# Optimization experiments

Measured on AMD Instinct MI355X. Metric: run time of the kernel, lower is better.

The kernel has to match this reference:

```python
import jax, jax.numpy as jnp
import numpy as np
from jax import lax

EPS_LN = 1e-5
EPS_NORM = 1e-12
NUM_HEADS = 8
KV_HEADS = 2
REP = NUM_HEADS // KV_HEADS


def _layernorm_c(x, w, b):
    # WithBias LayerNorm over channel dim; x: [b,c,h,w]
    mu = x.mean(axis=1, keepdims=True)
    var = ((x - mu) ** 2).mean(axis=1, keepdims=True)
    return (x - mu) / jnp.sqrt(var + EPS_LN) * w[None, :, None, None] + b[None, :, None, None]


def _conv1x1(x, w):
    # x: [b,c,h,w], w: [o,c]
    return jnp.einsum('bchw,oc->bohw', x, w)


def _dwconv3x3(x, w):
    # depthwise 3x3, SAME padding; w: [C,1,3,3]
    C = x.shape[1]
    return lax.conv_general_dilated(
        x, w, window_strides=(1, 1), padding='SAME',
        dimension_numbers=('NCHW', 'OIHW', 'NCHW'), feature_group_count=C)


def _l2norm(x):
    # normalize over last axis (torch F.normalize semantics)
    n = jnp.sqrt(jnp.sum(x * x, axis=-1, keepdims=True))
    return x / jnp.maximum(n, EPS_NORM)


def setup_inputs() -> dict:
    key = jax.random.key(0)
    ks = jax.random.split(key, 8)
    b, dim, h, w = 4, 192, 256, 256
    kv_ch = 2 * dim // REP  # 96
    return {
        'x': jax.random.normal(ks[0], (b, dim, h, w), jnp.float32),
        'ln_w': jnp.ones((dim,), jnp.float32),
        'ln_b': jnp.zeros((dim,), jnp.float32),
        'q_w': jax.random.normal(ks[1], (dim, dim), jnp.float32) * 0.02,
        'q_dw': jax.random.normal(ks[2], (dim, 1, 3, 3), jnp.float32) * 0.1,
        'kv_w': jax.random.normal(ks[3], (kv_ch, dim), jnp.float32) * 0.02,
        'kv_dw': jax.random.normal(ks[4], (kv_ch, 1, 3, 3), jnp.float32) * 0.1,
        'proj_w': jax.random.normal(ks[5], (dim, dim), jnp.float32) * 0.02,
        'temperature': jnp.ones((NUM_HEADS, 1, 1), jnp.float32),
    }


def reference(x, ln_w, ln_b, q_w, q_dw, kv_w, kv_dw, proj_w, temperature):
    b, c, h, w = x.shape
    xn = _layernorm_c(x, ln_w, ln_b)
    q = _dwconv3x3(_conv1x1(xn, q_w), q_dw)            # [b, c, h, w]
    kv = _dwconv3x3(_conv1x1(xn, kv_w), kv_dw)         # [b, 2c/rep, h, w]
    k, v = jnp.split(kv, 2, axis=1)
    hw = h * w
    ch = c // NUM_HEADS
    q = q.reshape(b, NUM_HEADS, ch, hw)
    k = k.reshape(b, KV_HEADS, ch, hw)
    v = v.reshape(b, KV_HEADS, ch, hw)
    k = jnp.repeat(k, REP, axis=1)                     # repeat_kv
    v = jnp.repeat(v, REP, axis=1)
    q = _l2norm(q)
    k = _l2norm(k)
    attn = jnp.einsum('bhcn,bhdn->bhcd', q, k) * temperature[None]
    attn = jax.nn.softmax(attn, axis=-1)
    out = jnp.einsum('bhcd,bhdn->bhcn', attn, v)
    out = out.reshape(b, c, h, w)
    return _conv1x1(out, proj_w)
```

## Files before the change

kernel.cpp:

```cpp
#include <hip/hip_runtime.h>
#include <hip/hip_bf16.h>
#include <stdint.h>

#define HW    65536
#define NB    4
#define CIN   192
#define OYC   288
#define BSTR  200

__device__ __forceinline__ float bflo(unsigned u){ return __uint_as_float(u << 16); }
__device__ __forceinline__ float bfhi(unsigned u){ return __uint_as_float(u & 0xffff0000u); }
__device__ __forceinline__ float bf2f(__hip_bfloat16 v){ return __bfloat162float(v); }
__device__ __forceinline__ unsigned short f2bfbits(float f){
  __hip_bfloat16 h = __float2bfloat16(f); return *(unsigned short*)&h;
}

__device__ __forceinline__ void unpack8(uint4 u, float* f) {
  f[0]=bflo(u.x); f[1]=bfhi(u.x); f[2]=bflo(u.y); f[3]=bfhi(u.y);
  f[4]=bflo(u.z); f[5]=bfhi(u.z); f[6]=bflo(u.w); f[7]=bfhi(u.w);
}

union BF8 { uint4 u; __hip_bfloat16 h[8]; };

typedef __attribute__((ext_vector_type(8))) short short8;
typedef __attribute__((ext_vector_type(4))) float floatx4;

__global__ void k_prep(const float* __restrict__ qw, const float* __restrict__ kvw,
                       const float* __restrict__ lnw, const float* __restrict__ lnb,
                       __hip_bfloat16* __restrict__ AF, float* __restrict__ bias) {
  int t = threadIdx.x;
  for (int i = t; i < OYC * CIN; i += 256) {
    int o = i / CIN, c = i % CIN;
    float w = (o < 192) ? qw[o * 192 + c] : kvw[(o - 192) * 192 + c];
    float val = w * lnw[c];
    int ot = o >> 4, lo = o & 15;
    int ks = c >> 5, cr = c & 31, q = cr >> 3, j = cr & 7;
    int dst = (((ot * 6 + ks) * 64) + q * 16 + lo) * 8 + j;
    AF[dst] = __float2bfloat16(val);
  }
  for (int o = t; o < OYC; o += 256) {
    float s = 0.f;
    for (int c = 0; c < CIN; ++c)
      s += ((o < 192) ? qw[o * 192 + c] : kvw[(o - 192) * 192 + c]) * lnb[c];
    bias[o] = s;
  }
}

__global__ __launch_bounds__(256, 4) void k_conv1(const float* __restrict__ x,
                                                  const __hip_bfloat16* __restrict__ AF,
                                                  const float* __restrict__ bias,
                                                  __hip_bfloat16* __restrict__ y) {
  __shared__ __align__(16) __hip_bfloat16 Bl[64 * BSTR];
  __shared__ float part[4][64][2];
  __shared__ float murs[64][2];
  __shared__ float biasl[OYC];
  int bid = blockIdx.x;
  int b  = bid >> 10;
  int n0 = (bid & 1023) * 64;
  int tid = threadIdx.x;
  int p = tid & 63, g = tid >> 6;

  for (int i = tid; i < OYC; i += 256) biasl[i] = bias[i];

  const float* xb = x + (size_t)(b * CIN + g * 48) * HW + n0 + p;
  float xv[48];
  float s = 0.f, ss = 0.f;
#pragma unroll
  for (int j = 0; j < 48; ++j) {
    float v = xb[(size_t)j * HW];
    xv[j] = v; s += v; ss += v * v;
  }
  part[g][p][0] = s; part[g][p][1] = ss;
  __syncthreads();
  if (tid < 64) {
    float s0 = 0.f, s1 = 0.f;
#pragma unroll
    for (int gg = 0; gg < 4; ++gg) { s0 += part[gg][tid][0]; s1 += part[gg][tid][1]; }
    float m = s0 * (1.f / CIN);
    float var = s1 * (1.f / CIN) - m * m;
    murs[tid][0] = m; murs[tid][1] = rsqrtf(var + 1e-5f);
  }
  __syncthreads();
  float mu = murs[p][0], rs = murs[p][1];
#pragma unroll
  for (int j = 0; j < 48; j += 2) {
    unsigned lo = f2bfbits((xv[j]     - mu) * rs);
    unsigned hi = f2bfbits((xv[j + 1] - mu) * rs);
    *(unsigned*)&Bl[p * BSTR + g * 48 + j] = lo | (hi << 16);
  }
  __syncthreads();

  int wave = tid >> 6, lane = tid & 63;
  int wo = wave >> 1, wn = wave & 1;
  int li = lane & 15, q = lane >> 4;

  floatx4 acc[9][2];
#pragma unroll
  for (int t = 0; t < 9; ++t)
#pragma unroll
    for (int nt = 0; nt < 2; ++nt) acc[t][nt] = (floatx4){0.f, 0.f, 0.f, 0.f};

  for (int ks = 0; ks < 6; ++ks) {
    short8 bf[2];
#pragma unroll
    for (int nt = 0; nt < 2; ++nt) {
      int pp = wn * 32 + nt * 16 + li;
      bf[nt] = *(const short8*)&Bl[pp * BSTR + ks * 32 + q * 8];
    }
    const __hip_bfloat16* ap = AF + (((wo * 9) * 6 + ks) * 64 + lane) * 8;
#pragma unroll
    for (int t = 0; t < 9; ++t) {
      short8 af = *(const short8*)(ap + t * 6 * 64 * 8);
      acc[t][0] = __builtin_amdgcn_mfma_f32_16x16x32_bf16(af, bf[0], acc[t][0], 0, 0, 0);
      acc[t][1] = __builtin_amdgcn_mfma_f32_16x16x32_bf16(af, bf[1], acc[t][1], 0, 0, 0);
    }
  }

#pragma unroll
  for (int t = 0; t < 9; ++t) {
#pragma unroll
    for (int nt = 0; nt < 2; ++nt) {
#pragma unroll
      for (int r = 0; r < 4; ++r) {
        int o = (wo * 9 + t) * 16 + q * 4 + r;
        int pp = wn * 32 + nt * 16 + li;
        y[(size_t)(b * OYC + o) * HW + n0 + pp] = __float2bfloat16(acc[t][nt][r] + biasl[o]);
      }
    }
  }
}

__global__ __launch_bounds__(256) void k_dwkv(const __hip_bfloat16* __restrict__ y,
                                              const float* __restrict__ kvdw,
                                              __hip_bfloat16* __restrict__ kbuf,
                                              __hip_bfloat16* __restrict__ vbuf,
                                              float* __restrict__ kss) {
  __shared__ __align__(16) __hip_bfloat16 stage[18 * 256];
  int bid = blockIdx.x;
  int hb = bid & 15;
  int ck = (bid >> 4) % 96;
  int b  = bid / (16 * 96);
  int tid = threadIdx.x;
  int h0 = hb * 16;

  const __hip_bfloat16* yp = y + (size_t)(b * OYC + 192 + ck) * HW;
  for (int i = tid; i < 18 * 32; i += 256) {
    int ry = i >> 5, seg = i & 31;
    int hh = h0 - 1 + ry;
    uint4 u = make_uint4(0u, 0u, 0u, 0u);
    if ((unsigned)hh < 256u) u = *(const uint4*)(yp + hh * 256 + seg * 8);
    *(uint4*)&stage[ry * 256 + seg * 8] = u;
  }
  __syncthreads();

  float w[9];
#pragma unroll
  for (int i = 0; i < 9; ++i) w[i] = kvdw[ck * 9 + i];

  int cg = tid & 31, rg = tid >> 5;
  int c0 = cg * 8;
  bool isk = (ck < 48);
  __hip_bfloat16* ob = (isk ? kbuf : vbuf) + (size_t)(b * 48 + (ck % 48)) * HW;
  float ssq = 0.f;
#pragma unroll
  for (int rr = 0; rr < 2; ++rr) {
    int orow = rg * 2 + rr;
    float o[8];
#pragma unroll
    for (int j = 0; j < 8; ++j) o[j] = 0.f;
#pragma unroll
    for (int ry = 0; ry < 3; ++ry) {
      const __hip_bfloat16* rb = &stage[(orow + ry) * 256];
      float v[8];
      unpack8(*(const uint4*)&rb[c0], v);
      float vl = (c0 > 0)       ? bf2f(rb[c0 - 1]) : 0.f;
      float vr = (c0 + 8 < 256) ? bf2f(rb[c0 + 8]) : 0.f;
      float wl = w[ry * 3], wm = w[ry * 3 + 1], wr = w[ry * 3 + 2];
      o[0] = fmaf(wl, vl, fmaf(wm, v[0], fmaf(wr, v[1], o[0])));
#pragma unroll
      for (int j = 1; j < 7; ++j)
        o[j] = fmaf(wl, v[j-1], fmaf(wm, v[j], fmaf(wr, v[j+1], o[j])));
      o[7] = fmaf(wl, v[6], fmaf(wm, v[7], fmaf(wr, vr, o[7])));
    }
    BF8 t;
#pragma unroll
    for (int j = 0; j < 8; ++j) {
      t.h[j] = __float2bfloat16(o[j]);
      if (isk) { float fv = bf2f(t.h[j]); ssq += fv * fv; }
    }
    *(uint4*)(ob + (size_t)(h0 + orow) * 256 + c0) = t.u;
  }
  if (isk) {
#pragma unroll
    for (int off = 32; off > 0; off >>= 1) ssq += __shfl_down(ssq, off);
    __shared__ float ws4[4];
    if ((tid & 63) == 0) ws4[tid >> 6] = ssq;
    __syncthreads();
    if (tid == 0) atomicAdd(&kss[b * 48 + ck], ws4[0] + ws4[1] + ws4[2] + ws4[3]);
  }
}

__global__ __launch_bounds__(256) void k_dwq(const __hip_bfloat16* __restrict__ y,
                                             const float* __restrict__ qdw,
                                             __hip_bfloat16* __restrict__ qfull,
                                             float* __restrict__ qss) {
  __shared__ __align__(16) __hip_bfloat16 stage[18 * 256];
  int bid = blockIdx.x;
  int hb = bid & 15;
  int c  = (bid >> 4) % 192;
  int b  = bid / (16 * 192);
  int tid = threadIdx.x;
  int h0 = hb * 16;

  const __hip_bfloat16* yp = y + (size_t)(b * OYC + c) * HW;
  for (int i = tid; i < 18 * 32; i += 256) {
    int ry = i >> 5, seg = i & 31;
    int hh = h0 - 1 + ry;
    uint4 u = make_uint4(0u, 0u, 0u, 0u);
    if ((unsigned)hh < 256u) u = *(const uint4*)(yp + hh * 256 + seg * 8);
    *(uint4*)&stage[ry * 256 + seg * 8] = u;
  }
  __syncthreads();

  float w[9];
#pragma unroll
  for (int i = 0; i < 9; ++i) w[i] = qdw[c * 9 + i];

  int cg = tid & 31, rg = tid >> 5;
  int c0 = cg * 8;
  __hip_bfloat16* ob = qfull + (size_t)(b * CIN + c) * HW;
  float ssq = 0.f;
#pragma unroll
  for (int rr = 0; rr < 2; ++rr) {
    int orow = rg * 2 + rr;
    float o[8];
#pragma unroll
    for (int j = 0; j < 8; ++j) o[j] = 0.f;
#pragma unroll
    for (int ry = 0; ry < 3; ++ry) {
      const __hip_bfloat16* rb = &stage[(orow + ry) * 256];
      float v[8];
      unpack8(*(const uint4*)&rb[c0], v);
      float vl = (c0 > 0)       ? bf2f(rb[c0 - 1]) : 0.f;
      float vr = (c0 + 8 < 256) ? bf2f(rb[c0 + 8]) : 0.f;
      float wl = w[ry * 3], wm = w[ry * 3 + 1], wr = w[ry * 3 + 2];
      o[0] = fmaf(wl, vl, fmaf(wm, v[0], fmaf(wr, v[1], o[0])));
#pragma unroll
      for (int j = 1; j < 7; ++j)
        o[j] = fmaf(wl, v[j-1], fmaf(wm, v[j], fmaf(wr, v[j+1], o[j])));
      o[7] = fmaf(wl, v[6], fmaf(wm, v[7], fmaf(wr, vr, o[7])));
    }
    BF8 t;
#pragma unroll
    for (int j = 0; j < 8; ++j) {
      t.h[j] = __float2bfloat16(o[j]);
      float fv = bf2f(t.h[j]); ssq += fv * fv;
    }
    *(uint4*)(ob + (size_t)(h0 + orow) * 256 + c0) = t.u;
  }
#pragma unroll
  for (int off = 32; off > 0; off >>= 1) ssq += __shfl_down(ssq, off);
  __shared__ float ws4[4];
  if ((tid & 63) == 0) ws4[tid >> 6] = ssq;
  __syncthreads();
  if (tid == 0) atomicAdd(&qss[b * 192 + c], ws4[0] + ws4[1] + ws4[2] + ws4[3]);
}

__global__ __launch_bounds__(256) void k_qk(const __hip_bfloat16* __restrict__ qfull,
                                            const __hip_bfloat16* __restrict__ kbuf,
                                            float* __restrict__ attn) {
  __shared__ float red[96 * 33];
  int bid = blockIdx.x;
  int ck  = bid & 63;
  int kvh = (bid >> 6) & 1;
  int b   = bid >> 7;
  int tid = threadIdx.x;
  int wave = tid >> 6, lane = tid & 63;
  int li = lane & 15, qd = lane >> 4;

  for (int i = tid; i < 96 * 33; i += 256) red[i] = 0.f;

  const __hip_bfloat16* qp = qfull + (size_t)(b * CIN + kvh * 96) * HW;
  const __hip_bfloat16* kp = kbuf  + (size_t)(b * 48 + kvh * 24) * HW;
  int n0 = ck * 1024 + wave * 256;

  floatx4 acc[6][2];
#pragma unroll
  for (int mt = 0; mt < 6; ++mt) {
    acc[mt][0] = (floatx4){0.f, 0.f, 0.f, 0.f};
    acc[mt][1] = (floatx4){0.f, 0.f, 0.f, 0.f};
  }

  int kr1 = 16 + li; if (kr1 > 23) kr1 = 23;
  for (int ks = 0; ks < 8; ++ks) {
    int nn = n0 + ks * 32 + qd * 8;
    short8 bk0 = *(const short8*)(kp + (size_t)li  * HW + nn);
    short8 bk1 = *(const short8*)(kp + (size_t)kr1 * HW + nn);
#pragma unroll
    for (int mt = 0; mt < 6; ++mt) {
      short8 aq = *(const short8*)(qp + (size_t)(mt * 16 + li) * HW + nn);
      acc[mt][0] = __builtin_amdgcn_mfma_f32_16x16x32_bf16(aq, bk0, acc[mt][0], 0, 0, 0);
      acc[mt][1] = __builtin_amdgcn_mfma_f32_16x16x32_bf16(aq, bk1, acc[mt][1], 0, 0, 0);
    }
  }
  __syncthreads();

#pragma unroll
  for (int mt = 0; mt < 6; ++mt) {
#pragma unroll
    for (int nt = 0; nt < 2; ++nt) {
      int n = nt * 16 + li;
      if (n < 24) {
#pragma unroll
        for (int r = 0; r < 4; ++r) {
          int m = mt * 16 + qd * 4 + r;
          atomicAdd(&red[m * 33 + n], acc[mt][nt][r]);
        }
      }
    }
  }
  __syncthreads();

  for (int i = tid; i < 96 * 24; i += 256) {
    int m = i / 24, d = i % 24;
    int head = kvh * 4 + m / 24, cp = m % 24;
    atomicAdd(&attn[(((b * 8 + head) * 24) + cp) * 24 + d], red[m * 33 + d]);
  }
}

__global__ void k_attn_final(const float* __restrict__ attn, const float* __restrict__ qss,
                             const float* __restrict__ kss, const float* __restrict__ temp,
                             const float* __restrict__ projw, float* __restrict__ Mt) {
  int b = blockIdx.x;
  int t = threadIdx.x;
  __shared__ float as_[96 * 25];
  float acc[48];
#pragma unroll
  for (int j = 0; j < 48; ++j) acc[j] = 0.f;
  for (int kvh = 0; kvh < 2; ++kvh) {
    __syncthreads();
    if (t < 96) {
      int row = kvh * 96 + t;
      int h = row / 24, cp = row % 24;
      float rq = 1.f / fmaxf(sqrtf(qss[b * 192 + row]), 1e-12f);
      float tp = temp[h];
      float lg[24]; float mx = -1e30f;
#pragma unroll
      for (int d = 0; d < 24; ++d) {
        float rk = 1.f / fmaxf(sqrtf(kss[b * 48 + kvh * 24 + d]), 1e-12f);
        float l = attn[(((b * 8 + h) * 24) + cp) * 24 + d] * rq * rk * tp;
        lg[d] = l; mx = fmaxf(mx, l);
      }
      float s = 0.f;
#pragma unroll
      for (int d = 0; d < 24; ++d) { lg[d] = __expf(lg[d] - mx); s += lg[d]; }
      float inv = 1.f / s;
#pragma unroll
      for (int d = 0; d < 24; ++d) as_[t * 25 + d] = lg[d] * inv;
    }
    __syncthreads();
    if (t < 192) {
      for (int cc = 0; cc < 96; ++cc) {
        float pw = projw[t * 192 + kvh * 96 + cc];
        const float* ar = &as_[cc * 25];
#pragma unroll
        for (int d = 0; d < 24; ++d) acc[kvh * 24 + d] = fmaf(pw, ar[d], acc[kvh * 24 + d]);
      }
    }
  }
  if (t < 192) {
#pragma unroll
    for (int j = 0; j < 48; ++j) Mt[((size_t)b * 48 + j) * 192 + t] = acc[j];
  }
}

__global__ __launch_bounds__(256) void k_out(const __hip_bfloat16* __restrict__ vbuf,
                                             const float* __restrict__ Mt,
                                             float* __restrict__ out) {
  __shared__ float lv[48 * 64];
  int bid = blockIdx.x;
  int b  = bid >> 10;
  int n0 = (bid & 1023) * 64;
  int tid = threadIdx.x;
  const __hip_bfloat16* vb = vbuf + (size_t)b * 48 * HW + n0;
  for (int i = tid; i < 48 * 64; i += 256) {
    int c = i >> 6, tn = i & 63;
    lv[i] = bf2f(vb[(size_t)c * HW + tn]);
  }
  __syncthreads();
  int wave = __builtin_amdgcn_readfirstlane(tid >> 6);
  int tn = tid & 63;
  const float* mb = Mt + (size_t)b * 48 * 192;
  for (int ch = 0; ch < 2; ++ch) {
    int o0 = wave * 48 + ch * 24;
    float acc[24];
#pragma unroll
    for (int j = 0; j < 24; ++j) acc[j] = 0.f;
    for (int c = 0; c < 48; ++c) {
      float xv = lv[c * 64 + tn];
#pragma unroll
      for (int j = 0; j < 24; ++j) acc[j] = fmaf(mb[c * 192 + o0 + j], xv, acc[j]);
    }
    float* op = out + ((size_t)b * 192 + o0) * HW + n0 + tn;
#pragma unroll
    for (int j = 0; j < 24; ++j) op[(size_t)j * HW] = acc[j];
  }
}

extern "C" void kernel_launch(void* const* d_in, const int* in_sizes, int n_in,
                              void* d_out, int out_size, void* d_ws, size_t ws_size,
                              hipStream_t stream) {
  const float* x     = (const float*)d_in[0];
  const float* ln_w  = (const float*)d_in[1];
  const float* ln_b  = (const float*)d_in[2];
  const float* q_w   = (const float*)d_in[3];
  const float* q_dw  = (const float*)d_in[4];
  const float* kv_w  = (const float*)d_in[5];
  const float* kv_dw = (const float*)d_in[6];
  const float* projw = (const float*)d_in[7];
  const float* temp  = (const float*)d_in[8];
  float* out = (float*)d_out;
  float* wsf = (float*)d_ws;

  float* qss  = wsf;
  float* kss  = wsf + 768;
  float* attn = wsf + 960;
  float* Mt   = wsf + 19392;
  float* bias = wsf + 56256;
  __hip_bfloat16* AF = (__hip_bfloat16*)(wsf + 56544);
  __hip_bfloat16* y    = (__hip_bfloat16*)(wsf + 111872);
  __hip_bfloat16* kbuf = (__hip_bfloat16*)(wsf + 37860608);
  __hip_bfloat16* vbuf = (__hip_bfloat16*)(wsf + 44152064);
  __hip_bfloat16* qfull = (__hip_bfloat16*)d_out;

  hipMemsetAsync(wsf, 0, 19392 * sizeof(float), stream);
  hipLaunchKernelGGL(k_prep, dim3(1), dim3(256), 0, stream, q_w, kv_w, ln_w, ln_b, AF, bias);
  hipLaunchKernelGGL(k_conv1, dim3(NB * 1024), dim3(256), 0, stream, x, AF, bias, y);
  hipLaunchKernelGGL(k_dwkv, dim3(NB * 96 * 16), dim3(256), 0, stream, y, kv_dw, kbuf, vbuf, kss);
  hipLaunchKernelGGL(k_dwq, dim3(NB * 192 * 16), dim3(256), 0, stream, y, q_dw, qfull, qss);
  hipLaunchKernelGGL(k_qk, dim3(NB * 2 * 64), dim3(256), 0, stream, qfull, kbuf, attn);
  hipLaunchKernelGGL(k_attn_final, dim3(NB), dim3(256), 0, stream, attn, qss, kss, temp, projw, Mt);
  hipLaunchKernelGGL(k_out, dim3(NB * 1024), dim3(256), 0, stream, vbuf, Mt, out);
}
```

Baseline: 679.9 us.

## Parallelize prep, prefetch A fragments, stage conv1 epilogue in LDS, widen k_out

k_prep now runs across 33 blocks instead of one. k_conv1 double-buffers the A-fragment loads across k-steps, and its epilogue goes through shared memory so y is written as 16-byte coalesced rows rather than scattered 2-byte stores. k_out now handles 256 pixels per block, with vectorized bf16 loads, four pixels per thread and float4 output stores. The aim is to cut serial prep latency and uncoalesced global stores, at the cost of more registers and extra syncs in k_conv1.

```diff
diff --git a/kernel.cpp b/kernel.cpp
--- a/kernel.cpp
+++ b/kernel.cpp
@@ -7,6 +7,7 @@
 #define CIN   192
 #define OYC   288
 #define BSTR  200
+#define EPS   72
 
 __device__ __forceinline__ float bflo(unsigned u){ return __uint_as_float(u << 16); }
 __device__ __forceinline__ float bfhi(unsigned u){ return __uint_as_float(u & 0xffff0000u); }
@@ -28,21 +29,24 @@
 __global__ void k_prep(const float* __restrict__ qw, const float* __restrict__ kvw,
                        const float* __restrict__ lnw, const float* __restrict__ lnb,
                        __hip_bfloat16* __restrict__ AF, float* __restrict__ bias) {
-  int t = threadIdx.x;
-  for (int i = t; i < OYC * CIN; i += 256) {
-    int o = i / CIN, c = i % CIN;
-    float w = (o < 192) ? qw[o * 192 + c] : kvw[(o - 192) * 192 + c];
-    float val = w * lnw[c];
-    int ot = o >> 4, lo = o & 15;
-    int ks = c >> 5, cr = c & 31, q = cr >> 3, j = cr & 7;
-    int dst = (((ot * 6 + ks) * 64) + q * 16 + lo) * 8 + j;
-    AF[dst] = __float2bfloat16(val);
-  }
-  for (int o = t; o < OYC; o += 256) {
-    float s = 0.f;
-    for (int c = 0; c < CIN; ++c)
-      s += ((o < 192) ? qw[o * 192 + c] : kvw[(o - 192) * 192 + c]) * lnb[c];
-    bias[o] = s;
+  int blk = blockIdx.x, t = threadIdx.x;
+  if (blk < 32) {
+    for (int i = blk * 256 + t; i < OYC * CIN; i += 32 * 256) {
+      int o = i / CIN, c = i % CIN;
+      float w = (o < 192) ? qw[o * 192 + c] : kvw[(o - 192) * 192 + c];
+      float val = w * lnw[c];
+      int ot = o >> 4, lo = o & 15;
+      int ks = c >> 5, cr = c & 31, q = cr >> 3, j = cr & 7;
+      int dst = (((ot * 6 + ks) * 64) + q * 16 + lo) * 8 + j;
+      AF[dst] = __float2bfloat16(val);
+    }
+  } else {
+    for (int o = t; o < OYC; o += 256) {
+      float s = 0.f;
+      for (int c = 0; c < CIN; ++c)
+        s += ((o < 192) ? qw[o * 192 + c] : kvw[(o - 192) * 192 + c]) * lnb[c];
+      bias[o] = s;
+    }
   }
 }
 
@@ -100,31 +104,54 @@
 #pragma unroll
     for (int nt = 0; nt < 2; ++nt) acc[t][nt] = (floatx4){0.f, 0.f, 0.f, 0.f};
 
+  const __hip_bfloat16* abase = AF + ((size_t)(wo * 9) * 6 * 64 + lane) * 8;
+  short8 a0[9], a1[9];
+#pragma unroll
+  for (int t = 0; t < 9; ++t) a0[t] = *(const short8*)(abase + (size_t)(t * 6) * 512);
+
+#pragma unroll
   for (int ks = 0; ks < 6; ++ks) {
-    short8 bf[2];
-#pragma unroll
-    for (int nt = 0; nt < 2; ++nt) {
-      int pp = wn * 32 + nt * 16 + li;
-      bf[nt] = *(const short8*)&Bl[pp * BSTR + ks * 32 + q * 8];
-    }
-    const __hip_bfloat16* ap = AF + (((wo * 9) * 6 + ks) * 64 + lane) * 8;
+    short8 bf0 = *(const short8*)&Bl[(wn * 32 + li) * BSTR + ks * 32 + q * 8];
+    short8 bf1 = *(const short8*)&Bl[(wn * 32 + 16 + li) * BSTR + ks * 32 + q * 8];
+    if (ks < 5) {
+#pragma unroll
+      for (int t = 0; t < 9; ++t) {
+        short8 v = *(const short8*)(abase + (size_t)(t * 6 + ks + 1) * 512);
+        if (ks & 1) a0[t] = v; else a1[t] = v;
+      }
+    }
 #pragma unroll
     for (int t = 0; t < 9; ++t) {
-      short8 af = *(const short8*)(ap + t * 6 * 64 * 8);
-      acc[t][0] = __builtin_amdgcn_mfma_f32_16x16x32_bf16(af, bf[0], acc[t][0], 0, 0, 0);
-      acc[t][1] = __builtin_amdgcn_mfma_f32_16x16x32_bf16(af, bf[1], acc[t][1], 0, 0, 0);
-    }
-  }
-
-#pragma unroll
-  for (int t = 0; t < 9; ++t) {
-#pragma unroll
-    for (int nt = 0; nt < 2; ++nt) {
-#pragma unroll
-      for (int r = 0; r < 4; ++r) {
-        int o = (wo * 9 + t) * 16 + q * 4 + r;
-        int pp = wn * 32 + nt * 16 + li;
-        y[(size_t)(b * OYC + o) * HW + n0 + pp] = __float2bfloat16(acc[t][nt][r] + biasl[o]);
+      short8 af = (ks & 1) ? a1[t] : a0[t];
+      acc[t][0] = __builtin_amdgcn_mfma_f32_16x16x32_bf16(af, bf0, acc[t][0], 0, 0, 0);
+      acc[t][1] = __builtin_amdgcn_mfma_f32_16x16x32_bf16(af, bf1, acc[t][1], 0, 0, 0);
+    }
+  }
+
+  __hip_bfloat16* EP = Bl;
+  int row = tid >> 3, cg8 = (tid & 7) * 8;
+#pragma unroll
+  for (int ph = 0; ph < 2; ++ph) {
+    __syncthreads();
+    if (wo == ph) {
+#pragma unroll
+      for (int t = 0; t < 9; ++t)
+#pragma unroll
+        for (int nt = 0; nt < 2; ++nt)
+#pragma unroll
+          for (int r = 0; r < 4; ++r) {
+            int orow = t * 16 + q * 4 + r;
+            int pp = wn * 32 + nt * 16 + li;
+            EP[orow * EPS + pp] = __float2bfloat16(acc[t][nt][r] + biasl[ph * 144 + orow]);
+          }
+    }
+    __syncthreads();
+#pragma unroll
+    for (int it = 0; it < 5; ++it) {
+      int rr = it * 32 + row;
+      if (rr < 144) {
+        uint4 u = *(const uint4*)&EP[rr * EPS + cg8];
+        *(uint4*)&y[(size_t)(b * OYC + ph * 144 + rr) * HW + n0 + cg8] = u;
       }
     }
   }
@@ -377,33 +404,47 @@
 __global__ __launch_bounds__(256) void k_out(const __hip_bfloat16* __restrict__ vbuf,
                                              const float* __restrict__ Mt,
                                              float* __restrict__ out) {
-  __shared__ float lv[48 * 64];
+  __shared__ __align__(16) __hip_bfloat16 lv[48 * 256];
   int bid = blockIdx.x;
-  int b  = bid >> 10;
-  int n0 = (bid & 1023) * 64;
+  int b  = bid >> 8;
+  int n0 = (bid & 255) * 256;
   int tid = threadIdx.x;
   const __hip_bfloat16* vb = vbuf + (size_t)b * 48 * HW + n0;
-  for (int i = tid; i < 48 * 64; i += 256) {
-    int c = i >> 6, tn = i & 63;
-    lv[i] = bf2f(vb[(size_t)c * HW + tn]);
-  }
-  __syncthreads();
-  int wave = __builtin_amdgcn_readfirstlane(tid >> 6);
-  int tn = tid & 63;
+  for (int i = tid; i < 48 * 32; i += 256) {
+    int c = i >> 5, seg = i & 31;
+    *(uint4*)&lv[c * 256 + seg * 8] = *(const uint4*)(vb + (size_t)c * HW + seg * 8);
+  }
+  __syncthreads();
+  int wave = tid >> 6, ln = tid & 63;
   const float* mb = Mt + (size_t)b * 48 * 192;
   for (int ch = 0; ch < 2; ++ch) {
     int o0 = wave * 48 + ch * 24;
-    float acc[24];
-#pragma unroll
-    for (int j = 0; j < 24; ++j) acc[j] = 0.f;
+    float acc[24][4];
+#pragma unroll
+    for (int j = 0; j < 24; ++j)
+#pragma unroll
+      for (int e = 0; e < 4; ++e) acc[j][e] = 0.f;
     for (int c = 0; c < 48; ++c) {
-      float xv = lv[c * 64 + tn];
-#pragma unroll
-      for (int j = 0; j < 24; ++j) acc[j] = fmaf(mb[c * 192 + o0 + j], xv, acc[j]);
-    }
-    float* op = out + ((size_t)b * 192 + o0) * HW + n0 + tn;
-#pragma unroll
-    for (int j = 0; j < 24; ++j) op[(size_t)j * HW] = acc[j];
+      float xv[4];
+      uint2 u = *(const uint2*)&lv[c * 256 + ln * 4];
+      xv[0] = bflo(u.x); xv[1] = bfhi(u.x); xv[2] = bflo(u.y); xv[3] = bfhi(u.y);
+      const float* mrow = mb + c * 192 + o0;
+      float4 m[6];
+#pragma unroll
+      for (int gg = 0; gg < 6; ++gg) m[gg] = *(const float4*)(mrow + gg * 4);
+      const float* mf = (const float*)&m[0];
+#pragma unroll
+      for (int j = 0; j < 24; ++j) {
+        float mv = mf[j];
+#pragma unroll
+        for (int e = 0; e < 4; ++e) acc[j][e] = fmaf(mv, xv[e], acc[j][e]);
+      }
+    }
+#pragma unroll
+    for (int j = 0; j < 24; ++j) {
+      float4 st = make_float4(acc[j][0], acc[j][1], acc[j][2], acc[j][3]);
+      *(float4*)&out[(size_t)(b * 192 + o0 + j) * HW + n0 + ln * 4] = st;
+    }
   }
 }
 
@@ -434,11 +475,11 @@
   __hip_bfloat16* qfull = (__hip_bfloat16*)d_out;
 
   hipMemsetAsync(wsf, 0, 19392 * sizeof(float), stream);
-  hipLaunchKernelGGL(k_prep, dim3(1), dim3(256), 0, stream, q_w, kv_w, ln_w, ln_b, AF, bias);
+  hipLaunchKernelGGL(k_prep, dim3(33), dim3(256), 0, stream, q_w, kv_w, ln_w, ln_b, AF, bias);
   hipLaunchKernelGGL(k_conv1, dim3(NB * 1024), dim3(256), 0, stream, x, AF, bias, y);
   hipLaunchKernelGGL(k_dwkv, dim3(NB * 96 * 16), dim3(256), 0, stream, y, kv_dw, kbuf, vbuf, kss);
   hipLaunchKernelGGL(k_dwq, dim3(NB * 192 * 16), dim3(256), 0, stream, y, q_dw, qfull, qss);
   hipLaunchKernelGGL(k_qk, dim3(NB * 2 * 64), dim3(256), 0, stream, qfull, kbuf, attn);
   hipLaunchKernelGGL(k_attn_final, dim3(NB), dim3(256), 0, stream, attn, qss, kss, temp, projw, Mt);
-  hipLaunchKernelGGL(k_out, dim3(NB * 1024), dim3(256), 0, stream, vbuf, Mt, out);
-}
+  hipLaunchKernelGGL(k_out, dim3(NB * 256), dim3(256), 0, stream, vbuf, Mt, out);
+}
```

Measured after the change: 664.3 us. 2.3% less time.
